# Kernel tuning notes

Measured on AMD Instinct MI355X. Metric: run time of the kernel, lower is better.

## Reference

```python
import jax, jax.numpy as jnp
import numpy as np

NUM_HEADS = 16
HEAD_SIZE = 64
MAX_POS = 2048  # config.max_position_embeddings


def setup_inputs() -> dict:
    key = jax.random.key(0)
    ks = jax.random.split(key, 8)
    B, Lq, Lk, D = 4, 1024, 2048, 1024
    s = 1.0 / np.sqrt(D)
    return {
        "hidden_states": jax.random.normal(ks[0], (B, Lk, D), jnp.float32),
        "query_hidden_states": jax.random.normal(ks[1], (B, Lq, D), jnp.float32),
        "attention_mask": jnp.zeros((B, 1, 1, Lk), jnp.float32),
        "Wq": jax.random.normal(ks[2], (D, D), jnp.float32) * s,
        "bq": jnp.zeros((D,), jnp.float32),
        "Wk": jax.random.normal(ks[3], (D, D), jnp.float32) * s,
        "bk": jnp.zeros((D,), jnp.float32),
        "Wv": jax.random.normal(ks[4], (D, D), jnp.float32) * s,
        "bv": jnp.zeros((D,), jnp.float32),
        "dist_emb": jax.random.normal(ks[5], (2 * MAX_POS - 1, HEAD_SIZE), jnp.float32) * 0.02,
    }


def _split_heads(x):
    # [B, L, H*Dh] -> [B, H, L, Dh]
    B, L, _ = x.shape
    return x.reshape(B, L, NUM_HEADS, HEAD_SIZE).transpose(0, 2, 1, 3)


def reference(hidden_states, query_hidden_states, attention_mask, Wq, bq, Wk, bk, Wv, bv, dist_emb):
    # Linear projections (torch Linear: x @ W.T + b)
    q = _split_heads(query_hidden_states @ Wq.T + bq)   # [B,H,Lq,Dh]
    k = _split_heads(hidden_states @ Wk.T + bk)          # [B,H,Lk,Dh]
    v = _split_heads(hidden_states @ Wv.T + bv)          # [B,H,Lk,Dh]

    scores = jnp.einsum('bhld,bhrd->bhlr', q, k)         # [B,H,Lq,Lk]

    # relative_key_query positional scores
    Lq, Lk = q.shape[2], k.shape[2]
    distance = jnp.arange(Lq)[:, None] - jnp.arange(Lk)[None, :]
    pe = dist_emb[distance + MAX_POS - 1]                # [Lq,Lk,Dh]
    scores = scores + jnp.einsum('bhld,lrd->bhlr', q, pe) + jnp.einsum('bhrd,lrd->bhlr', k, pe)

    scores = scores / np.sqrt(HEAD_SIZE) + attention_mask
    probs = jax.nn.softmax(scores, axis=-1)              # dropout p=0 (eval)
    ctx = jnp.einsum('bhlr,bhrd->bhld', probs, v)        # [B,H,Lq,Dh]
    B = ctx.shape[0]
    return ctx.transpose(0, 2, 1, 3).reshape(B, Lq, NUM_HEADS * HEAD_SIZE)
```

## Files before the change

kernel.cpp:

```cpp
#include <hip/hip_runtime.h>
#include <hip/hip_bf16.h>

#define B_   4
#define H_   16
#define LQ   1024
#define LK   2048
#define D_   1024
#define DH   64

typedef __attribute__((ext_vector_type(8))) short  short8;
typedef __attribute__((ext_vector_type(4))) float  float4_;
typedef __attribute__((ext_vector_type(4))) unsigned int uint4_;

static __device__ __forceinline__ float bf2f(unsigned short u) {
    unsigned int x = ((unsigned int)u) << 16;
    return __builtin_bit_cast(float, x);
}
static __device__ __forceinline__ unsigned short f2bf(float f) {
    unsigned int x = __builtin_bit_cast(unsigned int, f);
    unsigned int lsb = (x >> 16) & 1u;
    x += 0x7fffu + lsb;
    return (unsigned short)(x >> 16);
}
static __device__ __forceinline__ unsigned int pack2(float a, float b) {
    __hip_bfloat162 h = __float22bfloat162_rn(make_float2(a, b));
    unsigned int r;
    __builtin_memcpy(&r, &h, 4);
    return r;
}
template<int CTRL>
static __device__ __forceinline__ float dppmv(float x) {
    int i = __builtin_bit_cast(int, x);
    int r = __builtin_amdgcn_update_dpp(i, i, CTRL, 0xf, 0xf, false);
    return __builtin_bit_cast(float, r);
}

#define MFMA(a, b, c) __builtin_amdgcn_mfma_f32_16x16x32_bf16((a), (b), (c), 0, 0, 0)

#define GLOAD_LDS16(g, l) __builtin_amdgcn_global_load_lds( \
    (const __attribute__((address_space(1))) unsigned int*)(const void*)(g), \
    (__attribute__((address_space(3))) unsigned int*)(void*)(l), 16, 0, 0)

__global__ __launch_bounds__(256) void conv_kernel(
    const float* __restrict__ Wq, const float* __restrict__ Wk,
    const float* __restrict__ Wv, const float* __restrict__ Eg,
    const float* __restrict__ Xq, const float* __restrict__ Xk,
    unsigned short* __restrict__ cWq, unsigned short* __restrict__ cWk,
    unsigned short* __restrict__ cWv, unsigned short* __restrict__ cEb,
    unsigned short* __restrict__ cXq, unsigned short* __restrict__ cXk)
{
    int bid = blockIdx.x;
    const float* src; unsigned short* dst; int nch;
    if (bid < 512)       { src = Wq; dst = cWq;              nch = 131072;  }
    else if (bid < 1024) { src = Wk; dst = cWk; bid -= 512;  nch = 131072;  }
    else if (bid < 1536) { src = Wv; dst = cWv; bid -= 1024; nch = 131072;  }
    else if (bid < 1664) { src = Eg; dst = cEb; bid -= 1536; nch = 32760;   }
    else if (bid < 3712) { src = Xq; dst = cXq; bid -= 1664; nch = 524288;  }
    else                 { src = Xk; dst = cXk; bid -= 3712; nch = 1048576; }
    int ch = bid * 256 + threadIdx.x;
    if (ch >= nch) return;
    const float* s = src + (size_t)ch * 8;
    float4_ v0 = *(const float4_*)s, v1 = *(const float4_*)(s + 4);
    uint4_ o;
    o[0] = pack2(v0[0], v0[1]); o[1] = pack2(v0[2], v0[3]);
    o[2] = pack2(v1[0], v1[1]); o[3] = pack2(v1[2], v1[3]);
    *(uint4_*)(dst + (size_t)ch * 8) = o;
}

__global__ __launch_bounds__(256) void proj_kernel(
    const unsigned short* __restrict__ Xq, const unsigned short* __restrict__ Xk,
    const unsigned short* __restrict__ Wq, const float* __restrict__ bq,
    const unsigned short* __restrict__ Wk, const float* __restrict__ bk,
    const unsigned short* __restrict__ Wv, const float* __restrict__ bv,
    unsigned short* __restrict__ Qh, unsigned short* __restrict__ Kh,
    unsigned short* __restrict__ VT)
{
    __shared__ short smem[32768];
    short* A0 = smem;
    short* B0 = smem + 8192;
    short* A1 = smem + 16384;
    short* B1 = smem + 24576;
    short* Cs = smem;

    int bid = blockIdx.x;
    int which, tm, tn;
    const unsigned short *X; const float* bias; const unsigned short* W;
    if (bid < 256)      { which = 0; int t = bid;       tm = t >> 3; tn = t & 7; X = Xq; W = Wq; bias = bq; }
    else if (bid < 768) { which = 1; int t = bid - 256; tm = t >> 3; tn = t & 7; X = Xk; W = Wk; bias = bk; }
    else                { which = 2; int t = bid - 768; tm = t >> 3; tn = t & 7; X = Xk; W = Wv; bias = bv; }

    int tid  = threadIdx.x;
    int wave = tid >> 6, lane = tid & 63;
    int wr = (wave >> 1) * 64, wc = (wave & 1) * 64;
    int m0 = tm * 128, n0 = tn * 128;

    float4_ acc[4][4];
    for (int a = 0; a < 4; ++a) for (int c = 0; c < 4; ++c) acc[a][c] = (float4_)0.0f;

    int rl = lane >> 3;
    int chs = (lane & 7) ^ rl;
    const unsigned short* Asrc = X + (size_t)(m0 + wave * 32 + rl) * D_ + (chs << 3);
    const unsigned short* Bsrc = W + (size_t)(n0 + wave * 32 + rl) * D_ + (chs << 3);

    int lrow = lane & 15, lk8 = (lane >> 4) * 8;
    int swz = lane & 7;

    auto stage = [&](short* Ad, short* Bd, int kt) {
        int k0 = kt * 64;
        #pragma unroll
        for (int c = 0; c < 4; ++c) {
            GLOAD_LDS16(Asrc + (size_t)(c * 8) * D_ + k0, &Ad[(wave * 32 + c * 8) * 64]);
            GLOAD_LDS16(Bsrc + (size_t)(c * 8) * D_ + k0, &Bd[(wave * 32 + c * 8) * 64]);
        }
    };
    auto compute = [&](const short* Aa, const short* Bb) {
        #pragma unroll
        for (int kk = 0; kk < 64; kk += 32) {
            int cgrp = (kk + lk8) >> 3;
            int coff = ((cgrp ^ swz) << 3);
            short8 af[4], bfr[4];
            #pragma unroll
            for (int rt = 0; rt < 4; ++rt)
                af[rt]  = *(const short8*)(&Aa[(wr + rt * 16 + lrow) * 64 + coff]);
            #pragma unroll
            for (int ct = 0; ct < 4; ++ct)
                bfr[ct] = *(const short8*)(&Bb[(wc + ct * 16 + lrow) * 64 + coff]);
            #pragma unroll
            for (int rt = 0; rt < 4; ++rt)
                #pragma unroll
                for (int ct = 0; ct < 4; ++ct)
                    acc[rt][ct] = MFMA(af[rt], bfr[ct], acc[rt][ct]);
        }
    };

    stage(A0, B0, 0);
    __syncthreads();
    for (int kt = 0; kt < 16; kt += 2) {
        if (kt + 1 < 16) stage(A1, B1, kt + 1);
        compute(A0, B0);
        __syncthreads();
        if (kt + 2 < 16) stage(A0, B0, kt + 2);
        compute(A1, B1);
        __syncthreads();
    }

    int lrow4 = (lane >> 4) * 4, lcol = lane & 15;
    if (which < 2) {
        int lsh = (which == 0) ? 10 : 11;
        int Lm1 = (1 << lsh) - 1;
        unsigned short* dst = (which == 0) ? Qh : Kh;
        for (int rt = 0; rt < 4; ++rt)
            for (int ct = 0; ct < 4; ++ct)
                for (int i = 0; i < 4; ++i) {
                    int m = m0 + wr + rt * 16 + lrow4 + i;
                    int n = n0 + wc + ct * 16 + lcol;
                    float v = acc[rt][ct][i] + bias[n];
                    int b = m >> lsh, s = m & Lm1;
                    int h = n >> 6, d = n & 63;
                    dst[((size_t)((b * H_ + h) << lsh) + (size_t)s) * DH + d] = f2bf(v);
                }
    } else {
        for (int rt = 0; rt < 4; ++rt)
            for (int ct = 0; ct < 4; ++ct)
                for (int i = 0; i < 4; ++i) {
                    int rl2 = wr + rt * 16 + lrow4 + i;
                    int cl  = wc + ct * 16 + lcol;
                    float v = acc[rt][ct][i] + bias[n0 + cl];
                    Cs[cl * 136 + rl2] = (short)f2bf(v);
                }
        __syncthreads();
        int b = m0 >> 11, r0 = m0 & 2047;
        int c = tid >> 1, half = tid & 1;
        int n = n0 + c, h = n >> 6, d = n & 63;
        unsigned short* dstp = VT + ((size_t)(b * H_ + h) * DH + d) * LK + r0 + half * 64;
        for (int j = 0; j < 8; ++j) {
            uint4_ v = *(const uint4_*)(&Cs[c * 136 + half * 64 + j * 8]);
            *(uint4_*)(dstp + j * 8) = v;
        }
    }
}

__global__ __launch_bounds__(256, 2) void attn_kernel(
    const unsigned short* __restrict__ Qh, const unsigned short* __restrict__ Kh,
    const unsigned short* __restrict__ VT, const unsigned short* __restrict__ Eb,
    const float* __restrict__ mask, float* __restrict__ out)
{
    __shared__ short smem[29312];
    short* Gs = smem + 16384;
    unsigned int* Gqk = (unsigned int*)(smem + 16384);
    short* Ps = smem + 24704;

    int bid = blockIdx.x;
    int l0 = (bid & 15) * 64;
    int bh = bid >> 4;
    int b  = bh >> 4, h = bh & 15;
    int tid = threadIdx.x, wave = tid >> 6, lane = tid & 63;
    int lr = lane & 15, lk8 = (lane >> 4) * 8, lr4 = (lane >> 4) * 4;
    int rl8 = lane >> 3;
    int sch = ((lane & 7) ^ rl8) << 3;
    int co0 = ((lane >> 4) ^ (lr & 7)) << 3;

    const unsigned short* Kbase = Kh + (size_t)bh * LK * DH;
    const unsigned short* Vbase = VT + (size_t)bh * DH * LK;

    #pragma unroll
    for (int c = 0; c < 2; ++c) {
        int rw = c * 32 + wave * 8;
        GLOAD_LDS16(Qh + ((size_t)(bh * LQ + l0 + rw + rl8)) * DH + sch,
                    &smem[rw * 64]);
    }
    __syncthreads();
    short8 aq0 = *(const short8*)(&smem[(wave * 16 + lr) * 64 + co0]);
    short8 aq1 = *(const short8*)(&smem[(wave * 16 + lr) * 64 + (co0 ^ 32)]);
    __syncthreads();

    auto stage_kv = [&](int nit, int buf) {
        int r0_ = nit * 64;
        short* Kb = smem + buf * 8192;
        short* Vb = smem + 4096 + buf * 8192;
        #pragma unroll
        for (int c = 0; c < 2; ++c) {
            int rw = c * 32 + wave * 8;
            GLOAD_LDS16(Kbase + (size_t)(r0_ + rw + rl8) * DH + sch, &Kb[rw * 64]);
            GLOAD_LDS16(Vbase + (size_t)(rw + rl8) * LK + r0_ + sch, &Vb[rw * 64]);
        }
    };
    stage_kv(0, 0);

    float m_i[4], l_i[4];
    float4_ Oacc[4];
    for (int i = 0; i < 4; ++i) { m_i[i] = -1e30f; l_i[i] = 0.f; Oacc[i] = (float4_)0.f; }

    short8 ef[8][2];
    {
        const unsigned short* ep = Eb + (size_t)(l0 + 1984 + lr) * DH + lk8;
        #pragma unroll
        for (int t = 0; t < 8; ++t) {
            ef[t][0] = *(const short8*)(ep + (size_t)t * 16 * DH);
            ef[t][1] = *(const short8*)(ep + (size_t)t * 16 * DH + 32);
        }
    }
    __syncthreads();

    for (int it2 = 0; it2 < 32; it2 += 2) {
      #pragma unroll
      for (int sub = 0; sub < 2; ++sub) {
        const int it = it2 + sub;
        const int p4 = sub * 4;
        int r0 = it * 64;
        const int cur = sub;
        const short* Kb = smem + cur * 8192;
        const short* Vb = smem + 4096 + cur * 8192;

        if (it < 31) stage_kv(it + 1, cur ^ 1);

        short8 ak0, ak1;
        float4_ Sacc[4];
        #pragma unroll
        for (int c = 0; c < 4; ++c) {
            short8 b0 = *(const short8*)(&Kb[(c * 16 + lr) * 64 + co0]);
            short8 b1 = *(const short8*)(&Kb[(c * 16 + lr) * 64 + (co0 ^ 32)]);
            float4_ s = (float4_)0.f;
            s = MFMA(aq0, b0, s);
            s = MFMA(aq1, b1, s);
            Sacc[c] = s;
            if (c == 0 || c == wave) { ak0 = b0; ak1 = b1; }
        }

        #pragma unroll
        for (int t = 0; t < 8; ++t) {
            int dq = t - wave, dk = t - 3 + wave;
            bool needq = (unsigned)dq < 5u, needk = (unsigned)dk < 5u;
            if (!(needq || needk)) continue;
            short8 e0 = ef[t ^ p4][0], e1 = ef[t ^ p4][1];
            int u = t * 16 + lr;
            if (needq) {
                float4_ g = (float4_)0.f;
                g = MFMA(aq0, e0, g); g = MFMA(aq1, e1, g);
                unsigned int p0 = pack2(g[0], g[1]), p1 = pack2(g[2], g[3]);
                #pragma unroll
                for (int i = 0; i < 4; ++i) {
                    int row = wave * 16 + lr4 + i;
                    unsigned int w32 = (i >> 1) ? p1 : p0;
                    unsigned short vq = (unsigned short)((i & 1) ? (w32 >> 16) : (w32 & 0xffff));
                    int tr = row - u + 63;
                    if ((unsigned)tr < 64u)
                        Gs[(row * 65 + tr) * 2] = (short)vq;
                }
            }
            if (needk) {
                float4_ gg = (float4_)0.f;
                gg = MFMA(ak0, e0, gg); gg = MFMA(ak1, e1, gg);
                unsigned int q0 = pack2(gg[0], gg[1]), q1 = pack2(gg[2], gg[3]);
                #pragma unroll
                for (int i = 0; i < 4; ++i) {
                    int row = wave * 16 + lr4 + i;
                    unsigned int w32 = (i >> 1) ? q1 : q0;
                    unsigned short vk = (unsigned short)((i & 1) ? (w32 >> 16) : (w32 & 0xffff));
                    int tl = u + row - 63;
                    if ((unsigned)tl < 64u)
                        Gs[(tl * 65 + row) * 2 + 1] = (short)vk;
                }
            }
        }
        __syncthreads();

        if (it < 31) {
            const unsigned short* ep =
                Eb + (size_t)(l0 + 1984 - 64 * (it + 1) + lr) * DH + lk8;
            #pragma unroll
            for (int t = 0; t < 4; ++t) {
                ef[t ^ p4 ^ 4][0] = *(const short8*)(ep + (size_t)t * 16 * DH);
                ef[t ^ p4 ^ 4][1] = *(const short8*)(ep + (size_t)t * 16 * DH + 32);
            }
        }

        float mk[4];
        for (int c = 0; c < 4; ++c) mk[c] = mask[b * LK + r0 + c * 16 + lr];
        #pragma unroll
        for (int i = 0; i < 4; ++i) {
            int tl = wave * 16 + lr4 + i;
            const unsigned int* gr = Gqk + tl * 65 + lr;
            unsigned int gva[4];
            gva[0] = gr[0]; gva[1] = gr[16]; gva[2] = gr[32]; gva[3] = gr[48];
            float scv[4], mx = -1e30f;
            #pragma unroll
            for (int c = 0; c < 4; ++c) {
                float sq = bf2f((unsigned short)(gva[c] & 0xffff));
                float sk = bf2f((unsigned short)(gva[c] >> 16));
                float sc = (Sacc[c][i] + sq + sk) * 0.125f + mk[c];
                scv[c] = sc;
                mx = fmaxf(mx, sc);
            }
            mx = fmaxf(mx, dppmv<0xB1>(mx));
            mx = fmaxf(mx, dppmv<0x4E>(mx));
            mx = fmaxf(mx, dppmv<0x141>(mx));
            mx = fmaxf(mx, dppmv<0x140>(mx));
            float mnew = fmaxf(m_i[i], mx);
            float alpha = __expf(m_i[i] - mnew);
            m_i[i] = mnew;
            float e0 = __expf(scv[0] - mnew), e1 = __expf(scv[1] - mnew);
            float e2 = __expf(scv[2] - mnew), e3 = __expf(scv[3] - mnew);
            unsigned int p01 = pack2(e0, e1), p23 = pack2(e2, e3);
            float rs = bf2f((unsigned short)(p01 & 0xffff)) + bf2f((unsigned short)(p01 >> 16))
                     + bf2f((unsigned short)(p23 & 0xffff)) + bf2f((unsigned short)(p23 >> 16));
            rs += dppmv<0xB1>(rs);
            rs += dppmv<0x4E>(rs);
            rs += dppmv<0x141>(rs);
            rs += dppmv<0x140>(rs);
            l_i[i] = l_i[i] * alpha + rs;
            for (int nt = 0; nt < 4; ++nt) Oacc[nt][i] *= alpha;
            short* Pr = Ps + tl * 72;
            Pr[ 0 + lr] = (short)(unsigned short)(p01 & 0xffff);
            Pr[16 + lr] = (short)(unsigned short)(p01 >> 16);
            Pr[32 + lr] = (short)(unsigned short)(p23 & 0xffff);
            Pr[48 + lr] = (short)(unsigned short)(p23 >> 16);
        }
        const short* Pa = Ps + (wave * 16 + lr) * 72;
        short8 ap0 = *(const short8*)(Pa + lk8);
        short8 ap1 = *(const short8*)(Pa + 32 + lk8);
        #pragma unroll
        for (int nt = 0; nt < 4; ++nt) {
            short8 v0 = *(const short8*)(&Vb[(nt * 16 + lr) * 64 + co0]);
            short8 v1 = *(const short8*)(&Vb[(nt * 16 + lr) * 64 + (co0 ^ 32)]);
            Oacc[nt] = MFMA(ap0, v0, Oacc[nt]);
            Oacc[nt] = MFMA(ap1, v1, Oacc[nt]);
        }
        __syncthreads();
      }
    }

    for (int nt = 0; nt < 4; ++nt)
        for (int i = 0; i < 4; ++i) {
            int row = l0 + wave * 16 + lr4 + i;
            int col = h * 64 + nt * 16 + lr;
            out[(size_t)(b * LQ + row) * D_ + col] = Oacc[nt][i] / l_i[i];
        }
}

extern "C" void kernel_launch(void* const* d_in, const int* in_sizes, int n_in,
                              void* d_out, int out_size, void* d_ws, size_t ws_size,
                              hipStream_t stream) {
    (void)in_sizes; (void)n_in; (void)out_size; (void)ws_size;
    const float* Xk   = (const float*)d_in[0];
    const float* Xq   = (const float*)d_in[1];
    const float* mask = (const float*)d_in[2];
    const float* Wq   = (const float*)d_in[3];
    const float* bq   = (const float*)d_in[4];
    const float* Wk   = (const float*)d_in[5];
    const float* bk   = (const float*)d_in[6];
    const float* Wv   = (const float*)d_in[7];
    const float* bv   = (const float*)d_in[8];
    const float* Eg   = (const float*)d_in[9];

    unsigned short* Qh  = (unsigned short*)d_ws;
    unsigned short* Kh  = Qh  + (size_t)4194304;
    unsigned short* VT  = Kh  + (size_t)8388608;
    unsigned short* cWq = VT  + (size_t)8388608;
    unsigned short* cWk = cWq + (size_t)1048576;
    unsigned short* cWv = cWk + (size_t)1048576;
    unsigned short* cEb = cWv + (size_t)1048576;
    unsigned short* cXq = cEb + (size_t)262144;
    unsigned short* cXk = (unsigned short*)d_out;
    float* o = (float*)d_out;

    conv_kernel<<<7808, 256, 0, stream>>>(Wq, Wk, Wv, Eg, Xq, Xk,
                                          cWq, cWk, cWv, cEb, cXq, cXk);
    proj_kernel<<<1280, 256, 0, stream>>>(cXq, cXk, cWq, bq, cWk, bk, cWv, bv, Qh, Kh, VT);
    attn_kernel<<<1024, 256, 0, stream>>>(Qh, Kh, VT, cEb, mask, o);
}
```

Measured before the change: 438.7 us.

## Share K/V tiles across two query tiles per 512-thread attention block

The attention kernel now runs 512-thread blocks that each process two adjacent 64-row query tiles, sharing one staged K/V tile between them. Each tile keeps its own positional-score and probability buffers in LDS. This halves the number of blocks and the global/L2 traffic for K and V. In exchange, V drops from double to single buffering and is loaded at the start of each iteration, which exposes more load latency. LDS use per block also rises, which may limit occupancy.

New measurement: 492.4 us. +12.2%, slower.

```diff
diff --git a/kernel.cpp b/kernel.cpp
--- a/kernel.cpp
+++ b/kernel.cpp
@@ -180,33 +180,39 @@
     }
 }
 
-__global__ __launch_bounds__(256, 2) void attn_kernel(
+__global__ __launch_bounds__(512, 2) void attn_kernel(
     const unsigned short* __restrict__ Qh, const unsigned short* __restrict__ Kh,
     const unsigned short* __restrict__ VT, const unsigned short* __restrict__ Eb,
     const float* __restrict__ mask, float* __restrict__ out)
 {
-    __shared__ short smem[29312];
-    short* Gs = smem + 16384;
-    unsigned int* Gqk = (unsigned int*)(smem + 16384);
-    short* Ps = smem + 24704;
+    __shared__ short smem[38144];
+    short* Gs = smem + 12288;
+    unsigned int* Gqk = (unsigned int*)(smem + 12288);
+    short* Ps = smem + 28928;
 
     int bid = blockIdx.x;
-    int l0 = (bid & 15) * 64;
-    int bh = bid >> 4;
+    int l0base = (bid & 7) * 128;
+    int bh = bid >> 3;
     int b  = bh >> 4, h = bh & 15;
     int tid = threadIdx.x, wave = tid >> 6, lane = tid & 63;
+    int wv = wave & 3, tile = wave >> 2;
+    int l0 = l0base + tile * 64;
     int lr = lane & 15, lk8 = (lane >> 4) * 8, lr4 = (lane >> 4) * 4;
     int rl8 = lane >> 3;
     int sch = ((lane & 7) ^ rl8) << 3;
     int co0 = ((lane >> 4) ^ (lr & 7)) << 3;
 
+    unsigned int* Gq_t = Gqk + tile * 4160;
+    short* Gs_t = Gs + tile * 8320;
+    short* Ps_t = Ps + tile * 4608;
+
     const unsigned short* Kbase = Kh + (size_t)bh * LK * DH;
     const unsigned short* Vbase = VT + (size_t)bh * DH * LK;
 
     #pragma unroll
     for (int c = 0; c < 2; ++c) {
-        int rw = c * 32 + wave * 8;
-        GLOAD_LDS16(Qh + ((size_t)(bh * LQ + l0 + rw + rl8)) * DH + sch,
+        int rw = wave * 16 + c * 8;
+        GLOAD_LDS16(Qh + ((size_t)(bh * LQ + l0base + rw + rl8)) * DH + sch,
                     &smem[rw * 64]);
     }
     __syncthreads();
@@ -214,18 +220,17 @@
     short8 aq1 = *(const short8*)(&smem[(wave * 16 + lr) * 64 + (co0 ^ 32)]);
     __syncthreads();
 
-    auto stage_kv = [&](int nit, int buf) {
-        int r0_ = nit * 64;
-        short* Kb = smem + buf * 8192;
-        short* Vb = smem + 4096 + buf * 8192;
-        #pragma unroll
-        for (int c = 0; c < 2; ++c) {
-            int rw = c * 32 + wave * 8;
-            GLOAD_LDS16(Kbase + (size_t)(r0_ + rw + rl8) * DH + sch, &Kb[rw * 64]);
-            GLOAD_LDS16(Vbase + (size_t)(rw + rl8) * LK + r0_ + sch, &Vb[rw * 64]);
-        }
+    auto stage_K = [&](int nit, int buf) {
+        short* Kb = smem + buf * 4096;
+        int rw = wave * 8;
+        GLOAD_LDS16(Kbase + (size_t)(nit * 64 + rw + rl8) * DH + sch, &Kb[rw * 64]);
     };
-    stage_kv(0, 0);
+    auto stage_V = [&](int nit) {
+        short* Vb = smem + 8192;
+        int rw = wave * 8;
+        GLOAD_LDS16(Vbase + (size_t)(rw + rl8) * LK + nit * 64 + sch, &Vb[rw * 64]);
+    };
+    stage_K(0, 0);
 
     float m_i[4], l_i[4];
     float4_ Oacc[4];
@@ -248,11 +253,11 @@
         const int it = it2 + sub;
         const int p4 = sub * 4;
         int r0 = it * 64;
-        const int cur = sub;
-        const short* Kb = smem + cur * 8192;
-        const short* Vb = smem + 4096 + cur * 8192;
-
-        if (it < 31) stage_kv(it + 1, cur ^ 1);
+        const short* Kb = smem + sub * 4096;
+        const short* Vb = smem + 8192;
+
+        if (it < 31) stage_K(it + 1, sub ^ 1);
+        stage_V(it);
 
         short8 ak0, ak1;
         float4_ Sacc[4];
@@ -264,12 +269,12 @@
             s = MFMA(aq0, b0, s);
             s = MFMA(aq1, b1, s);
             Sacc[c] = s;
-            if (c == 0 || c == wave) { ak0 = b0; ak1 = b1; }
+            if (c == 0 || c == wv) { ak0 = b0; ak1 = b1; }
         }
 
         #pragma unroll
         for (int t = 0; t < 8; ++t) {
-            int dq = t - wave, dk = t - 3 + wave;
+            int dq = t - wv, dk = t - 3 + wv;
             bool needq = (unsigned)dq < 5u, needk = (unsigned)dk < 5u;
             if (!(needq || needk)) continue;
             short8 e0 = ef[t ^ p4][0], e1 = ef[t ^ p4][1];
@@ -280,12 +285,12 @@
                 unsigned int p0 = pack2(g[0], g[1]), p1 = pack2(g[2], g[3]);
                 #pragma unroll
                 for (int i = 0; i < 4; ++i) {
-                    int row = wave * 16 + lr4 + i;
+                    int row = wv * 16 + lr4 + i;
                     unsigned int w32 = (i >> 1) ? p1 : p0;
                     unsigned short vq = (unsigned short)((i & 1) ? (w32 >> 16) : (w32 & 0xffff));
                     int tr = row - u + 63;
                     if ((unsigned)tr < 64u)
-                        Gs[(row * 65 + tr) * 2] = (short)vq;
+                        Gs_t[(row * 65 + tr) * 2] = (short)vq;
                 }
             }
             if (needk) {
@@ -294,12 +299,12 @@
                 unsigned int q0 = pack2(gg[0], gg[1]), q1 = pack2(gg[2], gg[3]);
                 #pragma unroll
                 for (int i = 0; i < 4; ++i) {
-                    int row = wave * 16 + lr4 + i;
+                    int row = wv * 16 + lr4 + i;
                     unsigned int w32 = (i >> 1) ? q1 : q0;
                     unsigned short vk = (unsigned short)((i & 1) ? (w32 >> 16) : (w32 & 0xffff));
                     int tl = u + row - 63;
                     if ((unsigned)tl < 64u)
-                        Gs[(tl * 65 + row) * 2 + 1] = (short)vk;
+                        Gs_t[(tl * 65 + row) * 2 + 1] = (short)vk;
                 }
             }
         }
@@ -319,8 +324,8 @@
         for (int c = 0; c < 4; ++c) mk[c] = mask[b * LK + r0 + c * 16 + lr];
         #pragma unroll
         for (int i = 0; i < 4; ++i) {
-            int tl = wave * 16 + lr4 + i;
-            const unsigned int* gr = Gqk + tl * 65 + lr;
+            int tl = wv * 16 + lr4 + i;
+            const unsigned int* gr = Gq_t + tl * 65 + lr;
             unsigned int gva[4];
             gva[0] = gr[0]; gva[1] = gr[16]; gva[2] = gr[32]; gva[3] = gr[48];
             float scv[4], mx = -1e30f;
@@ -350,13 +355,13 @@
             rs += dppmv<0x140>(rs);
             l_i[i] = l_i[i] * alpha + rs;
             for (int nt = 0; nt < 4; ++nt) Oacc[nt][i] *= alpha;
-            short* Pr = Ps + tl * 72;
+            short* Pr = Ps_t + tl * 72;
             Pr[ 0 + lr] = (short)(unsigned short)(p01 & 0xffff);
             Pr[16 + lr] = (short)(unsigned short)(p01 >> 16);
             Pr[32 + lr] = (short)(unsigned short)(p23 & 0xffff);
             Pr[48 + lr] = (short)(unsigned short)(p23 >> 16);
         }
-        const short* Pa = Ps + (wave * 16 + lr) * 72;
+        const short* Pa = Ps_t + (wv * 16 + lr) * 72;
         short8 ap0 = *(const short8*)(Pa + lk8);
         short8 ap1 = *(const short8*)(Pa + 32 + lk8);
         #pragma unroll
@@ -372,7 +377,7 @@
 
     for (int nt = 0; nt < 4; ++nt)
         for (int i = 0; i < 4; ++i) {
-            int row = l0 + wave * 16 + lr4 + i;
+            int row = l0 + wv * 16 + lr4 + i;
             int col = h * 64 + nt * 16 + lr;
             out[(size_t)(b * LQ + row) * D_ + col] = Oacc[nt][i] / l_i[i];
         }
@@ -407,5 +412,5 @@
     conv_kernel<<<7808, 256, 0, stream>>>(Wq, Wk, Wv, Eg, Xq, Xk,
                                           cWq, cWk, cWv, cEb, cXq, cXk);
     proj_kernel<<<1280, 256, 0, stream>>>(cXq, cXk, cWq, bq, cWk, bk, cWv, bv, Qh, Kh, VT);
-    attn_kernel<<<1024, 256, 0, stream>>>(Qh, Kh, VT, cEb, mask, o);
-}
+    attn_kernel<<<512, 512, 0, stream>>>(Qh, Kh, VT, cEb, mask, o);
+}
```
